# Kernel optimization log

Hardware: AMD Instinct MI355X
Metric: run time of the kernel (lower is better)

## Reference

```python
import jax, jax.numpy as jnp
import numpy as np

BETA = 0.0  # vcon_steps=0 -> beta=0 -> pure MAM (max+min); beta=1 would be standard GEMM


def setup_inputs() -> dict:
    key = jax.random.key(0)
    k1, k2, k3 = jax.random.split(key, 3)
    in_features, out_features = 512, 512
    x = jax.random.normal(k1, (8, 128, in_features), dtype=jnp.float32)
    # kaiming_uniform-ish scale for weight, uniform bound for bias
    bound_w = float(np.sqrt(1.0 / in_features))
    weight = jax.random.uniform(k2, (out_features, in_features), dtype=jnp.float32,
                                minval=-bound_w, maxval=bound_w)
    bias = jax.random.uniform(k3, (out_features,), dtype=jnp.float32,
                              minval=-bound_w, maxval=bound_w)
    return {"x": x, "weight": weight, "bias": bias}


def reference(x, weight, bias):
    # x: [..., K]; weight: [M, K]; bias: [M]
    K = x.shape[-1]
    xf = x.reshape(-1, K)                      # [N, K]
    # elementwise products per (row, input, output): [N, K, M]
    P = xf[:, :, None] * weight.T[None, :, :]
    pmax = jnp.max(P, axis=1)                  # [N, M]
    argmax = jnp.argmax(P, axis=1).astype(jnp.int32)
    pmin = jnp.min(P, axis=1)                  # [N, M]
    argmin = jnp.argmin(P, axis=1).astype(jnp.int32)
    mam = pmax + pmin
    if BETA > 0.0:
        full = jnp.einsum('nk,mk->nm', xf, weight)
        C_flat = mam + BETA * (full - mam) + bias
    else:
        C_flat = mam + bias
    C = C_flat.reshape(x.shape[:-1] + (weight.shape[0],))
    return C, argmax, argmin
```

## Files before the change

### kernel.cpp

```cpp
#include <hip/hip_runtime.h>
#include <math.h>


constexpr int NTOT = 1024;
constexpr int MTOT = 512;
constexpr int KTOT = 512;
constexpr int BN = 32;
constexpr int BM = 32;
constexpr int BK = 128;
constexpr int G  = 16;
constexpr int LDSP = BK + 4;

__device__ __forceinline__ float max3f(float a, float b, float c) {
  float d; asm("v_max3_f32 %0, %1, %2, %3" : "=v"(d) : "v"(a), "v"(b), "v"(c)); return d;
}
__device__ __forceinline__ float min3f(float a, float b, float c) {
  float d; asm("v_min3_f32 %0, %1, %2, %3" : "=v"(d) : "v"(a), "v"(b), "v"(c)); return d;
}
__device__ __forceinline__ float4 f4mul(float4 a, float4 b) {
  return make_float4(a.x * b.x, a.y * b.y, a.z * b.z, a.w * b.w);
}

#define CELL(S, A0, A1, A2, A3, B0, B1, B2, B3)                              \
  {                                                                          \
    const float4 q0 = f4mul(A0, B0), q1 = f4mul(A1, B1);                     \
    const float4 q2 = f4mul(A2, B2), q3 = f4mul(A3, B3);                     \
    const float M = fmaxf(max3f(max3f(q0.x, q0.y, q0.z),                     \
                                max3f(q0.w, q1.x, q1.y),                     \
                                max3f(q1.z, q1.w, q2.x)),                    \
                          max3f(max3f(q2.y, q2.z, q2.w), q3.x,               \
                                max3f(q3.y, q3.z, q3.w)));                   \
    const float m = fminf(min3f(min3f(q0.x, q0.y, q0.z),                     \
                                min3f(q0.w, q1.x, q1.y),                     \
                                min3f(q1.z, q1.w, q2.x)),                    \
                          min3f(min3f(q2.y, q2.z, q2.w), q3.x,               \
                                min3f(q3.y, q3.z, q3.w)));                   \
    const bool u = M > vmax##S;                                              \
    vmax##S = u ? M : vmax##S;  gx##S = u ? gk : gx##S;                      \
    const bool v = m < vmin##S;                                              \
    vmin##S = v ? m : vmin##S;  gn##S = v ? gk : gn##S;                      \
  }

__device__ __forceinline__ int find_first_eq(const float* __restrict__ xr,
                                             const float* __restrict__ wr,
                                             float tgt, int base) {
  const float4 a0 = *(const float4*)(xr + 0),  a1 = *(const float4*)(xr + 4);
  const float4 a2 = *(const float4*)(xr + 8),  a3 = *(const float4*)(xr + 12);
  const float4 b0 = *(const float4*)(wr + 0),  b1 = *(const float4*)(wr + 4);
  const float4 b2 = *(const float4*)(wr + 8),  b3 = *(const float4*)(wr + 12);
  int idx = base;
  idx = (a3.w * b3.w == tgt) ? base + 15 : idx;
  idx = (a3.z * b3.z == tgt) ? base + 14 : idx;
  idx = (a3.y * b3.y == tgt) ? base + 13 : idx;
  idx = (a3.x * b3.x == tgt) ? base + 12 : idx;
  idx = (a2.w * b2.w == tgt) ? base + 11 : idx;
  idx = (a2.z * b2.z == tgt) ? base + 10 : idx;
  idx = (a2.y * b2.y == tgt) ? base +  9 : idx;
  idx = (a2.x * b2.x == tgt) ? base +  8 : idx;
  idx = (a1.w * b1.w == tgt) ? base +  7 : idx;
  idx = (a1.z * b1.z == tgt) ? base +  6 : idx;
  idx = (a1.y * b1.y == tgt) ? base +  5 : idx;
  idx = (a1.x * b1.x == tgt) ? base +  4 : idx;
  idx = (a0.w * b0.w == tgt) ? base +  3 : idx;
  idx = (a0.z * b0.z == tgt) ? base +  2 : idx;
  idx = (a0.y * b0.y == tgt) ? base +  1 : idx;
  idx = (a0.x * b0.x == tgt) ? base +  0 : idx;
  return idx;
}

__global__ __launch_bounds__(256, 2) void mam_kernel(
    const float* __restrict__ X,
    const float* __restrict__ W,
    const float* __restrict__ B,
    float* __restrict__ out)
{
  __shared__ float sx[BN][LDSP];
  __shared__ float sw[BM][LDSP];

  const int t  = threadIdx.x;
  const int n0 = blockIdx.y * BN;
  const int m0 = blockIdx.x * BM;

  const int tn = t >> 4;
  const int tm = t & 15;
  const int r0 = tn, r1 = tn + 16;
  const int c0 = tm, c1 = tm + 16;

  float vmax00 = -INFINITY, vmax01 = -INFINITY, vmax10 = -INFINITY, vmax11 = -INFINITY;
  float vmin00 =  INFINITY, vmin01 =  INFINITY, vmin10 =  INFINITY, vmin11 =  INFINITY;
  int   gx00 = 0, gx01 = 0, gx10 = 0, gx11 = 0;
  int   gn00 = 0, gn01 = 0, gn10 = 0, gn11 = 0;

  #pragma unroll 1
  for (int kc = 0; kc < KTOT; kc += BK) {
    __syncthreads();
    #pragma unroll
    for (int j = 0; j < 4; ++j) {
      const int id = t + 256 * j;
      const int r  = id >> 5;
      const int f  = id & 31;
      *reinterpret_cast<float4*>(&sx[r][f * 4]) =
          *reinterpret_cast<const float4*>(&X[(n0 + r) * KTOT + kc + f * 4]);
      *reinterpret_cast<float4*>(&sw[r][f * 4]) =
          *reinterpret_cast<const float4*>(&W[(m0 + r) * KTOT + kc + f * 4]);
    }
    __syncthreads();

    #pragma unroll
    for (int g8 = 0; g8 < BK / G; ++g8) {
      const int gk = kc + g8 * G;
      const float4* xap = reinterpret_cast<const float4*>(&sx[r0][g8 * G]);
      const float4* xbp = reinterpret_cast<const float4*>(&sx[r1][g8 * G]);
      const float4* wap = reinterpret_cast<const float4*>(&sw[c0][g8 * G]);
      const float4* wbp = reinterpret_cast<const float4*>(&sw[c1][g8 * G]);
      const float4 xa0 = xap[0], xa1 = xap[1], xa2 = xap[2], xa3 = xap[3];
      const float4 xb0 = xbp[0], xb1 = xbp[1], xb2 = xbp[2], xb3 = xbp[3];
      const float4 wa0 = wap[0], wa1 = wap[1], wa2 = wap[2], wa3 = wap[3];
      const float4 wb0 = wbp[0], wb1 = wbp[1], wb2 = wbp[2], wb3 = wbp[3];

      CELL(00, xa0, xa1, xa2, xa3, wa0, wa1, wa2, wa3)
      CELL(01, xa0, xa1, xa2, xa3, wb0, wb1, wb2, wb3)
      CELL(10, xb0, xb1, xb2, xb3, wa0, wa1, wa2, wa3)
      CELL(11, xb0, xb1, xb2, xb3, wb0, wb1, wb2, wb3)
    }
  }

  const float* Xr0 = &X[(n0 + r0) * KTOT];
  const float* Xr1 = &X[(n0 + r1) * KTOT];
  const float* Wc0 = &W[(m0 + c0) * KTOT];
  const float* Wc1 = &W[(m0 + c1) * KTOT];

  const int imax00 = find_first_eq(Xr0 + gx00, Wc0 + gx00, vmax00, gx00);
  const int imin00 = find_first_eq(Xr0 + gn00, Wc0 + gn00, vmin00, gn00);
  const int imax01 = find_first_eq(Xr0 + gx01, Wc1 + gx01, vmax01, gx01);
  const int imin01 = find_first_eq(Xr0 + gn01, Wc1 + gn01, vmin01, gn01);
  const int imax10 = find_first_eq(Xr1 + gx10, Wc0 + gx10, vmax10, gx10);
  const int imin10 = find_first_eq(Xr1 + gn10, Wc0 + gn10, vmin10, gn10);
  const int imax11 = find_first_eq(Xr1 + gx11, Wc1 + gx11, vmax11, gx11);
  const int imin11 = find_first_eq(Xr1 + gn11, Wc1 + gn11, vmin11, gn11);

  float* Cout = out;
  float* AM   = out + NTOT * MTOT;
  float* AN   = AM + NTOT * MTOT;

  const float b0 = B[m0 + c0];
  const float b1 = B[m0 + c1];

  const int o00 = (n0 + r0) * MTOT + (m0 + c0);
  const int o01 = (n0 + r0) * MTOT + (m0 + c1);
  const int o10 = (n0 + r1) * MTOT + (m0 + c0);
  const int o11 = (n0 + r1) * MTOT + (m0 + c1);

  Cout[o00] = vmax00 + vmin00 + b0;  AM[o00] = (float)imax00;  AN[o00] = (float)imin00;
  Cout[o01] = vmax01 + vmin01 + b1;  AM[o01] = (float)imax01;  AN[o01] = (float)imin01;
  Cout[o10] = vmax10 + vmin10 + b0;  AM[o10] = (float)imax10;  AN[o10] = (float)imin10;
  Cout[o11] = vmax11 + vmin11 + b1;  AM[o11] = (float)imax11;  AN[o11] = (float)imin11;
}

extern "C" void kernel_launch(void* const* d_in, const int* in_sizes, int n_in,
                              void* d_out, int out_size, void* d_ws, size_t ws_size,
                              hipStream_t stream) {
  const float* X = (const float*)d_in[0];
  const float* W = (const float*)d_in[1];
  const float* B = (const float*)d_in[2];
  float* out = (float*)d_out;

  dim3 grid(MTOT / BM, NTOT / BN);
  mam_kernel<<<grid, dim3(256), 0, stream>>>(X, W, B, out);
}
```

Measured before the change: 35.10 us.

## Split K across two thread halves per block and merge via LDS

Doubles the block to 512 threads. Each half scans a different 64-wide slice of every 128-wide K chunk, and at the end the partial max/min and argmax/argmin results are merged through shared memory with first-index tie-breaking. This raises the number of waves per block to hide latency on a grid of only 512 blocks. It adds a merge step, extra barriers, and a 512-thread launch bound that may limit registers. Products are also computed with an inline v_fma_f32 with zero addend instead of a plain multiply.

```diff
diff --git a/kernel.cpp b/kernel.cpp
--- a/kernel.cpp
+++ b/kernel.cpp
@@ -17,8 +17,11 @@
 __device__ __forceinline__ float min3f(float a, float b, float c) {
   float d; asm("v_min3_f32 %0, %1, %2, %3" : "=v"(d) : "v"(a), "v"(b), "v"(c)); return d;
 }
+__device__ __forceinline__ float fmul0(float a, float b) {
+  float d; asm("v_fma_f32 %0, %1, %2, 0" : "=v"(d) : "v"(a), "v"(b)); return d;
+}
 __device__ __forceinline__ float4 f4mul(float4 a, float4 b) {
-  return make_float4(a.x * b.x, a.y * b.y, a.z * b.z, a.w * b.w);
+  return make_float4(fmul0(a.x, b.x), fmul0(a.y, b.y), fmul0(a.z, b.z), fmul0(a.w, b.w));
 }
 
 #define CELL(S, A0, A1, A2, A3, B0, B1, B2, B3)                              \
@@ -39,6 +42,19 @@
     vmax##S = u ? M : vmax##S;  gx##S = u ? gk : gx##S;                      \
     const bool v = m < vmin##S;                                              \
     vmin##S = v ? m : vmin##S;  gn##S = v ? gk : gn##S;                      \
+  }
+
+#define MERGE(S, RR, CC)                                                     \
+  {                                                                          \
+    const int cell = (RR) * 32 + (CC);                                       \
+    const float pmx = comb[cell * 4 + 0];                                    \
+    const int   pgx = __float_as_int(comb[cell * 4 + 1]);                    \
+    const float pmn = comb[cell * 4 + 2];                                    \
+    const int   pgn = __float_as_int(comb[cell * 4 + 3]);                    \
+    if (pmx > vmax##S) { vmax##S = pmx; gx##S = pgx; }                       \
+    else if (pmx == vmax##S && pgx < gx##S) { gx##S = pgx; }                 \
+    if (pmn < vmin##S) { vmin##S = pmn; gn##S = pgn; }                       \
+    else if (pmn == vmin##S && pgn < gn##S) { gn##S = pgn; }                 \
   }
 
 __device__ __forceinline__ int find_first_eq(const float* __restrict__ xr,
@@ -68,7 +84,7 @@
   return idx;
 }
 
-__global__ __launch_bounds__(256, 2) void mam_kernel(
+__global__ __launch_bounds__(512, 4) void mam_kernel(
     const float* __restrict__ X,
     const float* __restrict__ W,
     const float* __restrict__ B,
@@ -77,7 +93,9 @@
   __shared__ float sx[BN][LDSP];
   __shared__ float sw[BM][LDSP];
 
-  const int t  = threadIdx.x;
+  const int th   = threadIdx.x;
+  const int half = th >> 8;
+  const int t    = th & 255;
   const int n0 = blockIdx.y * BN;
   const int m0 = blockIdx.x * BM;
 
@@ -85,6 +103,7 @@
   const int tm = t & 15;
   const int r0 = tn, r1 = tn + 16;
   const int c0 = tm, c1 = tm + 16;
+  const int kbase = half * 64;
 
   float vmax00 = -INFINITY, vmax01 = -INFINITY, vmax10 = -INFINITY, vmax11 = -INFINITY;
   float vmin00 =  INFINITY, vmin01 =  INFINITY, vmin10 =  INFINITY, vmin11 =  INFINITY;
@@ -95,8 +114,8 @@
   for (int kc = 0; kc < KTOT; kc += BK) {
     __syncthreads();
     #pragma unroll
-    for (int j = 0; j < 4; ++j) {
-      const int id = t + 256 * j;
+    for (int j = 0; j < 2; ++j) {
+      const int id = th + 512 * j;
       const int r  = id >> 5;
       const int f  = id & 31;
       *reinterpret_cast<float4*>(&sx[r][f * 4]) =
@@ -107,12 +126,13 @@
     __syncthreads();
 
     #pragma unroll
-    for (int g8 = 0; g8 < BK / G; ++g8) {
-      const int gk = kc + g8 * G;
-      const float4* xap = reinterpret_cast<const float4*>(&sx[r0][g8 * G]);
-      const float4* xbp = reinterpret_cast<const float4*>(&sx[r1][g8 * G]);
-      const float4* wap = reinterpret_cast<const float4*>(&sw[c0][g8 * G]);
-      const float4* wbp = reinterpret_cast<const float4*>(&sw[c1][g8 * G]);
+    for (int g8 = 0; g8 < 4; ++g8) {
+      const int off = kbase + g8 * G;
+      const int gk  = kc + off;
+      const float4* xap = reinterpret_cast<const float4*>(&sx[r0][off]);
+      const float4* xbp = reinterpret_cast<const float4*>(&sx[r1][off]);
+      const float4* wap = reinterpret_cast<const float4*>(&sw[c0][off]);
+      const float4* wbp = reinterpret_cast<const float4*>(&sw[c1][off]);
       const float4 xa0 = xap[0], xa1 = xap[1], xa2 = xap[2], xa3 = xap[3];
       const float4 xb0 = xbp[0], xb1 = xbp[1], xb2 = xbp[2], xb3 = xbp[3];
       const float4 wa0 = wap[0], wa1 = wap[1], wa2 = wap[2], wa3 = wap[3];
@@ -125,36 +145,61 @@
     }
   }
 
-  const float* Xr0 = &X[(n0 + r0) * KTOT];
-  const float* Xr1 = &X[(n0 + r1) * KTOT];
-  const float* Wc0 = &W[(m0 + c0) * KTOT];
-  const float* Wc1 = &W[(m0 + c1) * KTOT];
-
-  const int imax00 = find_first_eq(Xr0 + gx00, Wc0 + gx00, vmax00, gx00);
-  const int imin00 = find_first_eq(Xr0 + gn00, Wc0 + gn00, vmin00, gn00);
-  const int imax01 = find_first_eq(Xr0 + gx01, Wc1 + gx01, vmax01, gx01);
-  const int imin01 = find_first_eq(Xr0 + gn01, Wc1 + gn01, vmin01, gn01);
-  const int imax10 = find_first_eq(Xr1 + gx10, Wc0 + gx10, vmax10, gx10);
-  const int imin10 = find_first_eq(Xr1 + gn10, Wc0 + gn10, vmin10, gn10);
-  const int imax11 = find_first_eq(Xr1 + gx11, Wc1 + gx11, vmax11, gx11);
-  const int imin11 = find_first_eq(Xr1 + gn11, Wc1 + gn11, vmin11, gn11);
-
-  float* Cout = out;
-  float* AM   = out + NTOT * MTOT;
-  float* AN   = AM + NTOT * MTOT;
-
-  const float b0 = B[m0 + c0];
-  const float b1 = B[m0 + c1];
-
-  const int o00 = (n0 + r0) * MTOT + (m0 + c0);
-  const int o01 = (n0 + r0) * MTOT + (m0 + c1);
-  const int o10 = (n0 + r1) * MTOT + (m0 + c0);
-  const int o11 = (n0 + r1) * MTOT + (m0 + c1);
-
-  Cout[o00] = vmax00 + vmin00 + b0;  AM[o00] = (float)imax00;  AN[o00] = (float)imin00;
-  Cout[o01] = vmax01 + vmin01 + b1;  AM[o01] = (float)imax01;  AN[o01] = (float)imin01;
-  Cout[o10] = vmax10 + vmin10 + b0;  AM[o10] = (float)imax10;  AN[o10] = (float)imin10;
-  Cout[o11] = vmax11 + vmin11 + b1;  AM[o11] = (float)imax11;  AN[o11] = (float)imin11;
+  __syncthreads();
+  float* comb = &sx[0][0];
+  if (half == 1) {
+    const int cells[4][2] = {{r0, c0}, {r0, c1}, {r1, c0}, {r1, c1}};
+    const float vals[4][2] = {{vmax00, vmin00}, {vmax01, vmin01},
+                              {vmax10, vmin10}, {vmax11, vmin11}};
+    const int gids[4][2] = {{gx00, gn00}, {gx01, gn01}, {gx10, gn10}, {gx11, gn11}};
+    #pragma unroll
+    for (int i = 0; i < 4; ++i) {
+      const int cell = cells[i][0] * 32 + cells[i][1];
+      comb[cell * 4 + 0] = vals[i][0];
+      comb[cell * 4 + 1] = __int_as_float(gids[i][0]);
+      comb[cell * 4 + 2] = vals[i][1];
+      comb[cell * 4 + 3] = __int_as_float(gids[i][1]);
+    }
+  }
+  __syncthreads();
+
+  if (half == 0) {
+    MERGE(00, r0, c0)
+    MERGE(01, r0, c1)
+    MERGE(10, r1, c0)
+    MERGE(11, r1, c1)
+
+    const float* Xr0 = &X[(n0 + r0) * KTOT];
+    const float* Xr1 = &X[(n0 + r1) * KTOT];
+    const float* Wc0 = &W[(m0 + c0) * KTOT];
+    const float* Wc1 = &W[(m0 + c1) * KTOT];
+
+    const int imax00 = find_first_eq(Xr0 + gx00, Wc0 + gx00, vmax00, gx00);
+    const int imin00 = find_first_eq(Xr0 + gn00, Wc0 + gn00, vmin00, gn00);
+    const int imax01 = find_first_eq(Xr0 + gx01, Wc1 + gx01, vmax01, gx01);
+    const int imin01 = find_first_eq(Xr0 + gn01, Wc1 + gn01, vmin01, gn01);
+    const int imax10 = find_first_eq(Xr1 + gx10, Wc0 + gx10, vmax10, gx10);
+    const int imin10 = find_first_eq(Xr1 + gn10, Wc0 + gn10, vmin10, gn10);
+    const int imax11 = find_first_eq(Xr1 + gx11, Wc1 + gx11, vmax11, gx11);
+    const int imin11 = find_first_eq(Xr1 + gn11, Wc1 + gn11, vmin11, gn11);
+
+    float* Cout = out;
+    float* AM   = out + NTOT * MTOT;
+    float* AN   = AM + NTOT * MTOT;
+
+    const float b0 = B[m0 + c0];
+    const float b1 = B[m0 + c1];
+
+    const int o00 = (n0 + r0) * MTOT + (m0 + c0);
+    const int o01 = (n0 + r0) * MTOT + (m0 + c1);
+    const int o10 = (n0 + r1) * MTOT + (m0 + c0);
+    const int o11 = (n0 + r1) * MTOT + (m0 + c1);
+
+    Cout[o00] = vmax00 + vmin00 + b0;  AM[o00] = (float)imax00;  AN[o00] = (float)imin00;
+    Cout[o01] = vmax01 + vmin01 + b1;  AM[o01] = (float)imax01;  AN[o01] = (float)imin01;
+    Cout[o10] = vmax10 + vmin10 + b0;  AM[o10] = (float)imax10;  AN[o10] = (float)imin10;
+    Cout[o11] = vmax11 + vmin11 + b1;  AM[o11] = (float)imax11;  AN[o11] = (float)imin11;
+  }
 }
 
 extern "C" void kernel_launch(void* const* d_in, const int* in_sizes, int n_in,
@@ -166,5 +211,5 @@
   float* out = (float*)d_out;
 
   dim3 grid(MTOT / BM, NTOT / BN);
-  mam_kernel<<<grid, dim3(256), 0, stream>>>(X, W, B, out);
-}
+  mam_kernel<<<grid, dim3(512), 0, stream>>>(X, W, B, out);
+}
```

Measured after the change: 32.61 us. -7.1%, faster.

## Split K across wave quarters with 4x4 register tiles and LDS merge

Applied to the files above, without the earlier changes.

Each thread now computes a 4x4 tile of output cells over one quarter of the K chunk instead of a 2x2 tile over the full chunk. The four quarter-partial max/min/argidx results are then combined through a shared-memory reduction that keeps the earliest index on ties. This raises register reuse of the LDS-loaded x and w vectors, cutting LDS traffic per product. The cost is more registers (likely lower occupancy), extra barriers and a merge epilogue. Products are also forced through an inline-asm v_fma_f32 with zero addend.

```diff
diff --git a/kernel.cpp b/kernel.cpp
--- a/kernel.cpp
+++ b/kernel.cpp
@@ -9,7 +9,7 @@
 constexpr int BM = 32;
 constexpr int BK = 128;
 constexpr int G  = 16;
-constexpr int LDSP = BK + 4;
+constexpr int LDSP = 132;
 
 __device__ __forceinline__ float max3f(float a, float b, float c) {
   float d; asm("v_max3_f32 %0, %1, %2, %3" : "=v"(d) : "v"(a), "v"(b), "v"(c)); return d;
@@ -17,29 +17,23 @@
 __device__ __forceinline__ float min3f(float a, float b, float c) {
   float d; asm("v_min3_f32 %0, %1, %2, %3" : "=v"(d) : "v"(a), "v"(b), "v"(c)); return d;
 }
+__device__ __forceinline__ float fmul0(float a, float b) {
+  float d; asm("v_fma_f32 %0, %1, %2, 0" : "=v"(d) : "v"(a), "v"(b)); return d;
+}
 __device__ __forceinline__ float4 f4mul(float4 a, float4 b) {
-  return make_float4(a.x * b.x, a.y * b.y, a.z * b.z, a.w * b.w);
-}
-
-#define CELL(S, A0, A1, A2, A3, B0, B1, B2, B3)                              \
-  {                                                                          \
-    const float4 q0 = f4mul(A0, B0), q1 = f4mul(A1, B1);                     \
-    const float4 q2 = f4mul(A2, B2), q3 = f4mul(A3, B3);                     \
-    const float M = fmaxf(max3f(max3f(q0.x, q0.y, q0.z),                     \
-                                max3f(q0.w, q1.x, q1.y),                     \
-                                max3f(q1.z, q1.w, q2.x)),                    \
-                          max3f(max3f(q2.y, q2.z, q2.w), q3.x,               \
-                                max3f(q3.y, q3.z, q3.w)));                   \
-    const float m = fminf(min3f(min3f(q0.x, q0.y, q0.z),                     \
-                                min3f(q0.w, q1.x, q1.y),                     \
-                                min3f(q1.z, q1.w, q2.x)),                    \
-                          min3f(min3f(q2.y, q2.z, q2.w), q3.x,               \
-                                min3f(q3.y, q3.z, q3.w)));                   \
-    const bool u = M > vmax##S;                                              \
-    vmax##S = u ? M : vmax##S;  gx##S = u ? gk : gx##S;                      \
-    const bool v = m < vmin##S;                                              \
-    vmin##S = v ? m : vmin##S;  gn##S = v ? gk : gn##S;                      \
-  }
+  return make_float4(fmul0(a.x, b.x), fmul0(a.y, b.y), fmul0(a.z, b.z), fmul0(a.w, b.w));
+}
+
+__device__ __forceinline__ void tree16(const float4& q0, const float4& q1,
+                                       const float4& q2, const float4& q3,
+                                       float& M, float& m) {
+  M = fmaxf(max3f(max3f(q0.x, q0.y, q0.z), max3f(q0.w, q1.x, q1.y),
+                  max3f(q1.z, q1.w, q2.x)),
+            max3f(max3f(q2.y, q2.z, q2.w), q3.x, max3f(q3.y, q3.z, q3.w)));
+  m = fminf(min3f(min3f(q0.x, q0.y, q0.z), min3f(q0.w, q1.x, q1.y),
+                  min3f(q1.z, q1.w, q2.x)),
+            min3f(min3f(q2.y, q2.z, q2.w), q3.x, min3f(q3.y, q3.z, q3.w)));
+}
 
 __device__ __forceinline__ int find_first_eq(const float* __restrict__ xr,
                                              const float* __restrict__ wr,
@@ -77,26 +71,30 @@
   __shared__ float sx[BN][LDSP];
   __shared__ float sw[BM][LDSP];
 
-  const int t  = threadIdx.x;
+  const int th      = threadIdx.x;
+  const int quarter = th >> 6;
+  const int t       = th & 63;
+  const int rb      = t >> 3;
+  const int cb      = t & 7;
   const int n0 = blockIdx.y * BN;
   const int m0 = blockIdx.x * BM;
 
-  const int tn = t >> 4;
-  const int tm = t & 15;
-  const int r0 = tn, r1 = tn + 16;
-  const int c0 = tm, c1 = tm + 16;
-
-  float vmax00 = -INFINITY, vmax01 = -INFINITY, vmax10 = -INFINITY, vmax11 = -INFINITY;
-  float vmin00 =  INFINITY, vmin01 =  INFINITY, vmin10 =  INFINITY, vmin11 =  INFINITY;
-  int   gx00 = 0, gx01 = 0, gx10 = 0, gx11 = 0;
-  int   gn00 = 0, gn01 = 0, gn10 = 0, gn11 = 0;
+  float vmax[4][4], vmin[4][4];
+  int   gx[4][4], gn[4][4];
+  #pragma unroll
+  for (int i = 0; i < 4; ++i)
+    #pragma unroll
+    for (int j = 0; j < 4; ++j) {
+      vmax[i][j] = -INFINITY; vmin[i][j] = INFINITY;
+      gx[i][j] = 0; gn[i][j] = 0;
+    }
 
   #pragma unroll 1
   for (int kc = 0; kc < KTOT; kc += BK) {
     __syncthreads();
     #pragma unroll
     for (int j = 0; j < 4; ++j) {
-      const int id = t + 256 * j;
+      const int id = th + 256 * j;
       const int r  = id >> 5;
       const int f  = id & 31;
       *reinterpret_cast<float4*>(&sx[r][f * 4]) =
@@ -107,54 +105,102 @@
     __syncthreads();
 
     #pragma unroll
-    for (int g8 = 0; g8 < BK / G; ++g8) {
-      const int gk = kc + g8 * G;
-      const float4* xap = reinterpret_cast<const float4*>(&sx[r0][g8 * G]);
-      const float4* xbp = reinterpret_cast<const float4*>(&sx[r1][g8 * G]);
-      const float4* wap = reinterpret_cast<const float4*>(&sw[c0][g8 * G]);
-      const float4* wbp = reinterpret_cast<const float4*>(&sw[c1][g8 * G]);
-      const float4 xa0 = xap[0], xa1 = xap[1], xa2 = xap[2], xa3 = xap[3];
-      const float4 xb0 = xbp[0], xb1 = xbp[1], xb2 = xbp[2], xb3 = xbp[3];
-      const float4 wa0 = wap[0], wa1 = wap[1], wa2 = wap[2], wa3 = wap[3];
-      const float4 wb0 = wbp[0], wb1 = wbp[1], wb2 = wbp[2], wb3 = wbp[3];
-
-      CELL(00, xa0, xa1, xa2, xa3, wa0, wa1, wa2, wa3)
-      CELL(01, xa0, xa1, xa2, xa3, wb0, wb1, wb2, wb3)
-      CELL(10, xb0, xb1, xb2, xb3, wa0, wa1, wa2, wa3)
-      CELL(11, xb0, xb1, xb2, xb3, wb0, wb1, wb2, wb3)
+    for (int g = 0; g < 2; ++g) {
+      const int off = quarter * 32 + g * G;
+      const int gk  = kc + off;
+      float4 xr[4][4];
+      #pragma unroll
+      for (int i = 0; i < 4; ++i)
+        #pragma unroll
+        for (int s = 0; s < 4; ++s)
+          xr[i][s] = *reinterpret_cast<const float4*>(&sx[rb + 8 * i][off + 4 * s]);
+
+      #pragma unroll
+      for (int j = 0; j < 4; ++j) {
+        float4 wv[4];
+        #pragma unroll
+        for (int s = 0; s < 4; ++s)
+          wv[s] = *reinterpret_cast<const float4*>(&sw[cb + 8 * j][off + 4 * s]);
+        #pragma unroll
+        for (int i = 0; i < 4; ++i) {
+          const float4 q0 = f4mul(xr[i][0], wv[0]);
+          const float4 q1 = f4mul(xr[i][1], wv[1]);
+          const float4 q2 = f4mul(xr[i][2], wv[2]);
+          const float4 q3 = f4mul(xr[i][3], wv[3]);
+          float M, m;
+          tree16(q0, q1, q2, q3, M, m);
+          const bool u = M > vmax[i][j];
+          vmax[i][j] = u ? M : vmax[i][j];  gx[i][j] = u ? gk : gx[i][j];
+          const bool v = m < vmin[i][j];
+          vmin[i][j] = v ? m : vmin[i][j];  gn[i][j] = v ? gk : gn[i][j];
+        }
+      }
     }
   }
 
-  const float* Xr0 = &X[(n0 + r0) * KTOT];
-  const float* Xr1 = &X[(n0 + r1) * KTOT];
-  const float* Wc0 = &W[(m0 + c0) * KTOT];
-  const float* Wc1 = &W[(m0 + c1) * KTOT];
-
-  const int imax00 = find_first_eq(Xr0 + gx00, Wc0 + gx00, vmax00, gx00);
-  const int imin00 = find_first_eq(Xr0 + gn00, Wc0 + gn00, vmin00, gn00);
-  const int imax01 = find_first_eq(Xr0 + gx01, Wc1 + gx01, vmax01, gx01);
-  const int imin01 = find_first_eq(Xr0 + gn01, Wc1 + gn01, vmin01, gn01);
-  const int imax10 = find_first_eq(Xr1 + gx10, Wc0 + gx10, vmax10, gx10);
-  const int imin10 = find_first_eq(Xr1 + gn10, Wc0 + gn10, vmin10, gn10);
-  const int imax11 = find_first_eq(Xr1 + gx11, Wc1 + gx11, vmax11, gx11);
-  const int imin11 = find_first_eq(Xr1 + gn11, Wc1 + gn11, vmin11, gn11);
+  __syncthreads();
+  float* combA = &sx[0][0];
+  float* combB = &sw[0][0];
+
+  auto write_part = [&](float* comb) {
+    #pragma unroll
+    for (int i = 0; i < 4; ++i)
+      #pragma unroll
+      for (int j = 0; j < 4; ++j) {
+        const int cell = (rb + 8 * i) * 32 + (cb + 8 * j);
+        float4 v = make_float4(vmax[i][j], __int_as_float(gx[i][j]),
+                               vmin[i][j], __int_as_float(gn[i][j]));
+        *reinterpret_cast<float4*>(&comb[cell * 4]) = v;
+      }
+  };
+  auto merge_part = [&](const float* comb) {
+    #pragma unroll
+    for (int i = 0; i < 4; ++i)
+      #pragma unroll
+      for (int j = 0; j < 4; ++j) {
+        const int cell = (rb + 8 * i) * 32 + (cb + 8 * j);
+        const float4 v = *reinterpret_cast<const float4*>(&comb[cell * 4]);
+        const float pmx = v.x;  const int pgx = __float_as_int(v.y);
+        const float pmn = v.z;  const int pgn = __float_as_int(v.w);
+        if (pmx > vmax[i][j]) { vmax[i][j] = pmx; gx[i][j] = pgx; }
+        else if (pmx == vmax[i][j] && pgx < gx[i][j]) { gx[i][j] = pgx; }
+        if (pmn < vmin[i][j]) { vmin[i][j] = pmn; gn[i][j] = pgn; }
+        else if (pmn == vmin[i][j] && pgn < gn[i][j]) { gn[i][j] = pgn; }
+      }
+  };
+
+  if (quarter == 2) write_part(combA);
+  if (quarter == 3) write_part(combB);
+  __syncthreads();
+  if (quarter == 0) merge_part(combA);
+  if (quarter == 1) merge_part(combB);
+  __syncthreads();
+  if (quarter == 1) write_part(combA);
+  __syncthreads();
+  if (quarter == 0) { merge_part(combA); write_part(combA); }
+  __syncthreads();
 
   float* Cout = out;
   float* AM   = out + NTOT * MTOT;
   float* AN   = AM + NTOT * MTOT;
 
-  const float b0 = B[m0 + c0];
-  const float b1 = B[m0 + c1];
-
-  const int o00 = (n0 + r0) * MTOT + (m0 + c0);
-  const int o01 = (n0 + r0) * MTOT + (m0 + c1);
-  const int o10 = (n0 + r1) * MTOT + (m0 + c0);
-  const int o11 = (n0 + r1) * MTOT + (m0 + c1);
-
-  Cout[o00] = vmax00 + vmin00 + b0;  AM[o00] = (float)imax00;  AN[o00] = (float)imin00;
-  Cout[o01] = vmax01 + vmin01 + b1;  AM[o01] = (float)imax01;  AN[o01] = (float)imin01;
-  Cout[o10] = vmax10 + vmin10 + b0;  AM[o10] = (float)imax10;  AN[o10] = (float)imin10;
-  Cout[o11] = vmax11 + vmin11 + b1;  AM[o11] = (float)imax11;  AN[o11] = (float)imin11;
+  #pragma unroll
+  for (int u = 0; u < 4; ++u) {
+    const int cell = th * 4 + u;
+    const float4 v = *reinterpret_cast<const float4*>(&combA[cell * 4]);
+    const float vmx = v.x;  const int gxc = __float_as_int(v.y);
+    const float vmn = v.z;  const int gnc = __float_as_int(v.w);
+    const int row = cell >> 5, col = cell & 31;
+    const int n = n0 + row, m = m0 + col;
+    const float* xr = &X[n * KTOT];
+    const float* wr = &W[m * KTOT];
+    const int imax = find_first_eq(xr + gxc, wr + gxc, vmx, gxc);
+    const int imin = find_first_eq(xr + gnc, wr + gnc, vmn, gnc);
+    const int o = n * MTOT + m;
+    Cout[o] = vmx + vmn + B[m];
+    AM[o] = (float)imax;
+    AN[o] = (float)imin;
+  }
 }
 
 extern "C" void kernel_launch(void* const* d_in, const int* in_sizes, int n_in,
```

After: 35.76 us. No clear change (+1.9%).

## Stage full W tile in LDS, read X from global with double-buffered registers

Applied to the files above, without the earlier changes.

The W tile now holds the whole K extent in shared memory and is loaded once. X rows are read straight from global memory (broadcast within a row group) instead of staged through LDS, with a two-set register double buffer so loads overlap the max/min compute. The K-loop barriers go away. Products now use an inline-asm FMA with zero so the compiler cannot fuse or reorder them. LDS use grows to about 66 KB per block, which may limit occupancy under launch_bounds(256,2), and register pressure rises from the double buffer.

```diff
diff --git a/kernel.cpp b/kernel.cpp
--- a/kernel.cpp
+++ b/kernel.cpp
@@ -7,9 +7,8 @@
 constexpr int KTOT = 512;
 constexpr int BN = 32;
 constexpr int BM = 32;
-constexpr int BK = 128;
 constexpr int G  = 16;
-constexpr int LDSP = BK + 4;
+constexpr int LDSPW = 516;
 
 __device__ __forceinline__ float max3f(float a, float b, float c) {
   float d; asm("v_max3_f32 %0, %1, %2, %3" : "=v"(d) : "v"(a), "v"(b), "v"(c)); return d;
@@ -17,28 +16,64 @@
 __device__ __forceinline__ float min3f(float a, float b, float c) {
   float d; asm("v_min3_f32 %0, %1, %2, %3" : "=v"(d) : "v"(a), "v"(b), "v"(c)); return d;
 }
+__device__ __forceinline__ float fmul0(float a, float b) {
+  float d; asm("v_fma_f32 %0, %1, %2, 0" : "=v"(d) : "v"(a), "v"(b)); return d;
+}
 __device__ __forceinline__ float4 f4mul(float4 a, float4 b) {
-  return make_float4(a.x * b.x, a.y * b.y, a.z * b.z, a.w * b.w);
+  return make_float4(fmul0(a.x, b.x), fmul0(a.y, b.y), fmul0(a.z, b.z), fmul0(a.w, b.w));
+}
+
+__device__ __forceinline__ void tree16(const float4& q0, const float4& q1,
+                                       const float4& q2, const float4& q3,
+                                       float& M, float& m) {
+  M = fmaxf(max3f(max3f(q0.x, q0.y, q0.z), max3f(q0.w, q1.x, q1.y),
+                  max3f(q1.z, q1.w, q2.x)),
+            max3f(max3f(q2.y, q2.z, q2.w), q3.x, max3f(q3.y, q3.z, q3.w)));
+  m = fminf(min3f(min3f(q0.x, q0.y, q0.z), min3f(q0.w, q1.x, q1.y),
+                  min3f(q1.z, q1.w, q2.x)),
+            min3f(min3f(q2.y, q2.z, q2.w), q3.x, min3f(q3.y, q3.z, q3.w)));
 }
 
 #define CELL(S, A0, A1, A2, A3, B0, B1, B2, B3)                              \
   {                                                                          \
     const float4 q0 = f4mul(A0, B0), q1 = f4mul(A1, B1);                     \
     const float4 q2 = f4mul(A2, B2), q3 = f4mul(A3, B3);                     \
-    const float M = fmaxf(max3f(max3f(q0.x, q0.y, q0.z),                     \
-                                max3f(q0.w, q1.x, q1.y),                     \
-                                max3f(q1.z, q1.w, q2.x)),                    \
-                          max3f(max3f(q2.y, q2.z, q2.w), q3.x,               \
-                                max3f(q3.y, q3.z, q3.w)));                   \
-    const float m = fminf(min3f(min3f(q0.x, q0.y, q0.z),                     \
-                                min3f(q0.w, q1.x, q1.y),                     \
-                                min3f(q1.z, q1.w, q2.x)),                    \
-                          min3f(min3f(q2.y, q2.z, q2.w), q3.x,               \
-                                min3f(q3.y, q3.z, q3.w)));                   \
+    float M, m;                                                              \
+    tree16(q0, q1, q2, q3, M, m);                                            \
     const bool u = M > vmax##S;                                              \
     vmax##S = u ? M : vmax##S;  gx##S = u ? gk : gx##S;                      \
     const bool v = m < vmin##S;                                              \
     vmin##S = v ? m : vmin##S;  gn##S = v ? gk : gn##S;                      \
+  }
+
+#define DECL_SET(S)                                                          \
+  float4 xa0##S, xa1##S, xa2##S, xa3##S, xb0##S, xb1##S, xb2##S, xb3##S;     \
+  float4 wa0##S, wa1##S, wa2##S, wa3##S, wb0##S, wb1##S, wb2##S, wb3##S;
+
+#define LOAD_SET(S, OFF)                                                     \
+  {                                                                          \
+    const int o_ = (OFF);                                                    \
+    xa0##S = *reinterpret_cast<const float4*>(Xr0 + o_ + 0);                 \
+    xa1##S = *reinterpret_cast<const float4*>(Xr0 + o_ + 4);                 \
+    xa2##S = *reinterpret_cast<const float4*>(Xr0 + o_ + 8);                 \
+    xa3##S = *reinterpret_cast<const float4*>(Xr0 + o_ + 12);                \
+    xb0##S = *reinterpret_cast<const float4*>(Xr1 + o_ + 0);                 \
+    xb1##S = *reinterpret_cast<const float4*>(Xr1 + o_ + 4);                 \
+    xb2##S = *reinterpret_cast<const float4*>(Xr1 + o_ + 8);                 \
+    xb3##S = *reinterpret_cast<const float4*>(Xr1 + o_ + 12);                \
+    const float4* wap_ = reinterpret_cast<const float4*>(&sw[c0][o_]);       \
+    wa0##S = wap_[0]; wa1##S = wap_[1]; wa2##S = wap_[2]; wa3##S = wap_[3];  \
+    const float4* wbp_ = reinterpret_cast<const float4*>(&sw[c1][o_]);       \
+    wb0##S = wbp_[0]; wb1##S = wbp_[1]; wb2##S = wbp_[2]; wb3##S = wbp_[3];  \
+  }
+
+#define COMP_SET(S, GK)                                                      \
+  {                                                                          \
+    const int gk = (GK);                                                     \
+    CELL(00, xa0##S, xa1##S, xa2##S, xa3##S, wa0##S, wa1##S, wa2##S, wa3##S) \
+    CELL(01, xa0##S, xa1##S, xa2##S, xa3##S, wb0##S, wb1##S, wb2##S, wb3##S) \
+    CELL(10, xb0##S, xb1##S, xb2##S, xb3##S, wa0##S, wa1##S, wa2##S, wa3##S) \
+    CELL(11, xb0##S, xb1##S, xb2##S, xb3##S, wb0##S, wb1##S, wb2##S, wb3##S) \
   }
 
 __device__ __forceinline__ int find_first_eq(const float* __restrict__ xr,
@@ -74,59 +109,46 @@
     const float* __restrict__ B,
     float* __restrict__ out)
 {
-  __shared__ float sx[BN][LDSP];
-  __shared__ float sw[BM][LDSP];
+  __shared__ float sw[BM][LDSPW];
 
-  const int t  = threadIdx.x;
+  const int th = threadIdx.x;
+  const int tn = th >> 4;
+  const int tm = th & 15;
   const int n0 = blockIdx.y * BN;
   const int m0 = blockIdx.x * BM;
-
-  const int tn = t >> 4;
-  const int tm = t & 15;
   const int r0 = tn, r1 = tn + 16;
   const int c0 = tm, c1 = tm + 16;
+
+  #pragma unroll
+  for (int j = 0; j < 16; ++j) {
+    const int id  = th + 256 * j;
+    const int row = id >> 7;
+    const int f   = id & 127;
+    *reinterpret_cast<float4*>(&sw[row][f * 4]) =
+        *reinterpret_cast<const float4*>(&W[(m0 + row) * KTOT + f * 4]);
+  }
+  __syncthreads();
+
+  const float* Xr0 = &X[(n0 + r0) * KTOT];
+  const float* Xr1 = &X[(n0 + r1) * KTOT];
 
   float vmax00 = -INFINITY, vmax01 = -INFINITY, vmax10 = -INFINITY, vmax11 = -INFINITY;
   float vmin00 =  INFINITY, vmin01 =  INFINITY, vmin10 =  INFINITY, vmin11 =  INFINITY;
   int   gx00 = 0, gx01 = 0, gx10 = 0, gx11 = 0;
   int   gn00 = 0, gn01 = 0, gn10 = 0, gn11 = 0;
 
-  #pragma unroll 1
-  for (int kc = 0; kc < KTOT; kc += BK) {
-    __syncthreads();
-    #pragma unroll
-    for (int j = 0; j < 4; ++j) {
-      const int id = t + 256 * j;
-      const int r  = id >> 5;
-      const int f  = id & 31;
-      *reinterpret_cast<float4*>(&sx[r][f * 4]) =
-          *reinterpret_cast<const float4*>(&X[(n0 + r) * KTOT + kc + f * 4]);
-      *reinterpret_cast<float4*>(&sw[r][f * 4]) =
-          *reinterpret_cast<const float4*>(&W[(m0 + r) * KTOT + kc + f * 4]);
-    }
-    __syncthreads();
+  DECL_SET(A)
+  DECL_SET(B_)
 
-    #pragma unroll
-    for (int g8 = 0; g8 < BK / G; ++g8) {
-      const int gk = kc + g8 * G;
-      const float4* xap = reinterpret_cast<const float4*>(&sx[r0][g8 * G]);
-      const float4* xbp = reinterpret_cast<const float4*>(&sx[r1][g8 * G]);
-      const float4* wap = reinterpret_cast<const float4*>(&sw[c0][g8 * G]);
-      const float4* wbp = reinterpret_cast<const float4*>(&sw[c1][g8 * G]);
-      const float4 xa0 = xap[0], xa1 = xap[1], xa2 = xap[2], xa3 = xap[3];
-      const float4 xb0 = xbp[0], xb1 = xbp[1], xb2 = xbp[2], xb3 = xbp[3];
-      const float4 wa0 = wap[0], wa1 = wap[1], wa2 = wap[2], wa3 = wap[3];
-      const float4 wb0 = wbp[0], wb1 = wbp[1], wb2 = wbp[2], wb3 = wbp[3];
-
-      CELL(00, xa0, xa1, xa2, xa3, wa0, wa1, wa2, wa3)
-      CELL(01, xa0, xa1, xa2, xa3, wb0, wb1, wb2, wb3)
-      CELL(10, xb0, xb1, xb2, xb3, wa0, wa1, wa2, wa3)
-      CELL(11, xb0, xb1, xb2, xb3, wb0, wb1, wb2, wb3)
-    }
+  LOAD_SET(A, 0)
+  #pragma unroll
+  for (int g = 0; g < 32; g += 2) {
+    LOAD_SET(B_, (g + 1) * G)
+    COMP_SET(A, g * G)
+    if (g + 2 < 32) LOAD_SET(A, (g + 2) * G)
+    COMP_SET(B_, (g + 1) * G)
   }
 
-  const float* Xr0 = &X[(n0 + r0) * KTOT];
-  const float* Xr1 = &X[(n0 + r1) * KTOT];
   const float* Wc0 = &W[(m0 + c0) * KTOT];
   const float* Wc1 = &W[(m0 + c1) * KTOT];
 
```

After: 93.27 us. +165.7%, slower.
